# Kernel optimization log

Hardware: AMD Instinct MI355X
Metric: run time of the kernel (lower is better)

Reference implementation:

```python
import jax, jax.numpy as jnp
import numpy as np

CH = 16
R = 9  # reduced_res = ceil(log2(256)+1)


def grid_sample_bilinear(P, gx, gy):
    """torch.F.grid_sample, mode=bilinear, align_corners=True, zeros padding.
    P: (C, H, W); gx indexes width (last axis), gy indexes height. Returns (C, N)."""
    C, H, W = P.shape
    ix = (gx + 1.0) * 0.5 * (W - 1)
    iy = (gy + 1.0) * 0.5 * (H - 1)
    x0 = jnp.floor(ix)
    y0 = jnp.floor(iy)
    wx = ix - x0
    wy = iy - y0
    x0i = jnp.clip(x0.astype(jnp.int32), 0, W - 1)
    x1i = jnp.clip(x0i + 1, 0, W - 1)
    y0i = jnp.clip(y0.astype(jnp.int32), 0, H - 1)
    y1i = jnp.clip(y0i + 1, 0, H - 1)
    v00 = P[:, y0i, x0i]
    v01 = P[:, y0i, x1i]
    v10 = P[:, y1i, x0i]
    v11 = P[:, y1i, x1i]
    return (v00 * (1 - wx) * (1 - wy) + v01 * wx * (1 - wy)
            + v10 * (1 - wx) * wy + v11 * wx * wy)


def plane_feature(P, gx, gy, c_int):
    # sample -> (N, ch, R), then cosine-basis numerical integration over R
    s = grid_sample_bilinear(P, gx, gy)              # (R*ch, N)
    s = s.T.reshape(-1, CH, R)                       # (N, ch, R)
    c = (c_int + 1.0) * 0.5 * (2.0 ** (R - 1) - 1.0)  # (N,)
    freqs = (2.0 ** jnp.arange(R, dtype=jnp.float32)) - 0.5
    basis = jnp.cos(jnp.pi * (c[:, None] + 0.5) * freqs / (2.0 ** R))  # (N, R)
    return 2.0 * jnp.einsum('nr,ncr->nc', basis, s)  # (N, ch)


def setup_inputs() -> dict:
    key = jax.random.key(0)
    k1, k2, k3, k4 = jax.random.split(key, 4)
    coords = jax.random.uniform(k1, (524288, 3), dtype=jnp.float32) * 2.0 - 1.0
    Pu = jax.random.normal(k2, (R * CH, 256, 256), dtype=jnp.float32) * 0.1
    Pv = jax.random.normal(k3, (R * CH, 256, 256), dtype=jnp.float32) * 0.1
    Pw = jax.random.normal(k4, (R * CH, 256, 256), dtype=jnp.float32) * 0.1
    return {"coords": coords, "Pu": Pu, "Pv": Pv, "Pw": Pw}


def reference(coords, Pu, Pv, Pw):
    # Pu sampled with (coord1, coord2), integrated along coord0; etc.
    fu = plane_feature(Pu, coords[:, 1], coords[:, 2], coords[:, 0])
    fv = plane_feature(Pv, coords[:, 0], coords[:, 2], coords[:, 1])
    fw = plane_feature(Pw, coords[:, 0], coords[:, 1], coords[:, 2])
    return fu + fv + fw  # (N, ch)
```

## Files before the change

### kernel.cpp

```cpp
#include <hip/hip_runtime.h>
#include <hip/hip_bf16.h>

#define CHN 16
#define RF 9
#define HWDIM 256
#define POSN (HWDIM * HWDIM)
#define NBINS 32768

typedef _Float16 half2_t __attribute__((ext_vector_type(2)));

__device__ __forceinline__ half2_t u2h(uint32_t u) {
    union { uint32_t u; half2_t h; } x; x.u = u; return x.h;
}
__device__ __forceinline__ uint32_t f2h(float f) {
    union { _Float16 h; uint16_t u; } x; x.h = (_Float16)f; return (uint32_t)x.u;
}
__device__ __forceinline__ float h2f(uint32_t u) {
    union { uint16_t u; _Float16 h; } x; x.u = (uint16_t)u; return (float)x.h;
}

#if __has_builtin(__builtin_amdgcn_fdot2)
__device__ __forceinline__ float DOT2(half2_t a, half2_t b, float c) {
    return __builtin_amdgcn_fdot2(a, b, c, false);
}
#else
__device__ __forceinline__ float DOT2(half2_t a, half2_t b, float c) {
    return fmaf((float)a.x, (float)b.x, fmaf((float)a.y, (float)b.y, c));
}
#endif

__device__ __forceinline__ uint32_t part1by2(uint32_t x) {
    x &= 0x3ffu;
    x = (x | (x << 16)) & 0x030000FFu;
    x = (x | (x << 8))  & 0x0300F00Fu;
    x = (x | (x << 4))  & 0x030C30C3u;
    x = (x | (x << 2))  & 0x09249249u;
    return x;
}
__device__ __forceinline__ uint32_t morton_key(float c0, float c1, float c2) {
    int q0 = min(31, max(0, (int)((c0 + 1.f) * 16.f)));
    int q1 = min(31, max(0, (int)((c1 + 1.f) * 16.f)));
    int q2 = min(31, max(0, (int)((c2 + 1.f) * 16.f)));
    return (part1by2((uint32_t)q0) << 2) | (part1by2((uint32_t)q1) << 1) | part1by2((uint32_t)q2);
}

__global__ __launch_bounds__(256) void prep_kernel(const float* __restrict__ Pu,
                                                   const float* __restrict__ Pv,
                                                   const float* __restrict__ Pw,
                                                   uint4* __restrict__ A,
                                                   uint32_t* __restrict__ B,
                                                   const float* __restrict__ coords,
                                                   uint32_t* __restrict__ hist,
                                                   int N, int tblk) {
    int b = blockIdx.x;
    if (b < tblk) {
        int tid = b * 256 + threadIdx.x;
        int pos = tid & (POSN - 1);
        int p = tid >> 16;
        const float* P = (p == 0) ? Pu : ((p == 1) ? Pv : Pw);
        uint32_t r8pk[8];
        uint4* Ap = A + ((size_t)p * POSN + pos) * CHN;
#pragma unroll
        for (int cc = 0; cc < CHN; ++cc) {
            const float* Pc = P + (size_t)(cc * RF) * POSN + pos;
            uint32_t w[4];
#pragma unroll
            for (int j = 0; j < 4; ++j) {
                float v0 = Pc[(size_t)(2 * j) * POSN];
                float v1 = Pc[(size_t)(2 * j + 1) * POSN];
                w[j] = f2h(v0) | (f2h(v1) << 16);
            }
            Ap[cc] = make_uint4(w[0], w[1], w[2], w[3]);
            uint32_t h8 = f2h(Pc[(size_t)8 * POSN]);
            if (cc & 1) r8pk[cc >> 1] |= (h8 << 16); else r8pk[cc >> 1] = h8;
        }
        uint32_t* Bp = B + ((size_t)p * POSN + pos) * 8;
#pragma unroll
        for (int j = 0; j < 8; ++j) Bp[j] = r8pk[j];
    } else {
        int n = (b - tblk) * 256 + threadIdx.x;
        if (n < N) {
            float c0 = coords[3 * n], c1 = coords[3 * n + 1], c2 = coords[3 * n + 2];
            atomicAdd(&hist[morton_key(c0, c1, c2)], 1u);
        }
    }
}

__global__ __launch_bounds__(1024) void scan_kernel(uint32_t* __restrict__ hist) {
    __shared__ uint32_t part[1024];
    int t = threadIdx.x;
    uint32_t loc[32];
    uint32_t s = 0;
    int base = t * 32;
#pragma unroll
    for (int i = 0; i < 32; ++i) { loc[i] = hist[base + i]; s += loc[i]; }
    part[t] = s;
    __syncthreads();
    for (int off = 1; off < 1024; off <<= 1) {
        uint32_t v = (t >= off) ? part[t - off] : 0u;
        __syncthreads();
        part[t] += v;
        __syncthreads();
    }
    uint32_t run = part[t] - s;
#pragma unroll
    for (int i = 0; i < 32; ++i) { hist[base + i] = run; run += loc[i]; }
}

__global__ __launch_bounds__(256) void scatter_kernel(const float* __restrict__ coords,
                                                      uint32_t* __restrict__ hist,
                                                      float4* __restrict__ sorted, int N) {
    int n = blockIdx.x * blockDim.x + threadIdx.x;
    if (n >= N) return;
    float c0 = coords[3 * n], c1 = coords[3 * n + 1], c2 = coords[3 * n + 2];
    uint32_t key = morton_key(c0, c1, c2);
    uint32_t dst = atomicAdd(&hist[key], 1u);
    sorted[dst] = make_float4(c0, c1, c2, __uint_as_float((uint32_t)n));
}

__global__ __launch_bounds__(256) void triplane_f16(const float4* __restrict__ sorted,
                                                    const uint4* __restrict__ A,
                                                    const uint32_t* __restrict__ B,
                                                    float* __restrict__ out, int N, int nblk) {
    __shared__ float4 pts[16];
    __shared__ uint32_t meta[16][3][16];
    int blk = blockIdx.x;
    if ((nblk & 7) == 0) {
        int cpx = nblk >> 3;
        blk = (blk & 7) * cpx + (blk >> 3);
    }
    int base = blk * 16;
    int t = threadIdx.x;
    if (t < 16) {
        int i = base + t;
        pts[t] = (i < N) ? sorted[i] : make_float4(0.f, 0.f, 0.f, __uint_as_float(0u));
    }
    __syncthreads();
    if (t < 64 && (t & 3) < 3) {
        int pt = t >> 2, p = t & 3;
        float4 c = pts[pt];
        float gx = (p == 0) ? c.y : c.x;
        float gy = (p == 2) ? c.y : c.z;
        float ci = (p == 0) ? c.x : ((p == 1) ? c.y : c.z);
        float ix = (gx + 1.f) * 127.5f;
        float iy = (gy + 1.f) * 127.5f;
        float x0f = floorf(ix), y0f = floorf(iy);
        float wx = ix - x0f, wy = iy - y0f;
        int x0 = min(max((int)x0f, 0), HWDIM - 1);
        int y0 = min(max((int)y0f, 0), HWDIM - 1);
        int x1 = min(x0 + 1, HWDIM - 1);
        int y1 = min(y0 + 1, HWDIM - 1);
        uint32_t* m = meta[pt][p];
        float cv = (ci + 1.f) * 127.5f + 0.5f;
        float bb[9];
#pragma unroll
        for (int r = 0; r < 9; ++r) {
            const float k = 3.14159265358979f * ((float)(1 << r) - 0.5f) * (1.f / 512.f);
            bb[r] = __cosf(cv * k);
        }
#pragma unroll
        for (int j = 0; j < 4; ++j) m[j] = f2h(bb[2 * j]) | (f2h(bb[2 * j + 1]) << 16);
        m[4] = __float_as_uint(bb[8]);
        m[5] = __float_as_uint((1.f - wx) * (1.f - wy));
        m[6] = __float_as_uint(wx * (1.f - wy));
        m[7] = __float_as_uint((1.f - wx) * wy);
        m[8] = __float_as_uint(wx * wy);
        m[9]  = (uint32_t)(y0 * HWDIM + x0) * 256u;
        m[10] = (uint32_t)(y0 * HWDIM + x1) * 256u;
        m[11] = (uint32_t)(y1 * HWDIM + x0) * 256u;
        m[12] = (uint32_t)(y1 * HWDIM + x1) * 256u;
    }
    __syncthreads();
    int pt = t >> 4, cc = t & 15;
    int gi = base + pt;
    if (gi >= N) return;
    float acc = 0.f;
    const char* Ab = (const char*)A;
    const char* Bb = (const char*)B;
#pragma unroll
    for (int p = 0; p < 3; ++p) {
        const uint32_t* m = meta[pt][p];
        half2_t b01 = u2h(m[0]), b23 = u2h(m[1]), b45 = u2h(m[2]), b67 = u2h(m[3]);
        float b8 = __uint_as_float(m[4]);
        const char* Apl = Ab + (size_t)p * ((size_t)POSN * 256);
        const char* Bpl = Bb + (size_t)p * ((size_t)POSN * 32);
        float ps = 0.f;
#pragma unroll
        for (int k = 0; k < 4; ++k) {
            uint32_t ob = m[9 + k];
            uint4 a = *(const uint4*)(Apl + ob + cc * 16);
            uint32_t bw = *(const uint32_t*)(Bpl + (ob >> 3) + ((cc >> 1) << 2));
            float v8 = h2f((cc & 1) ? (bw >> 16) : (bw & 0xffffu));
            float s = b8 * v8;
            s = DOT2(u2h(a.x), b01, s);
            s = DOT2(u2h(a.y), b23, s);
            s = DOT2(u2h(a.z), b45, s);
            s = DOT2(u2h(a.w), b67, s);
            ps = fmaf(__uint_as_float(m[5 + k]), s, ps);
        }
        acc += ps;
    }
    uint32_t n = __float_as_uint(pts[pt].w);
    out[(size_t)n * CHN + cc] = 2.f * acc;
}

__global__ __launch_bounds__(256) void triplane_direct(const float* __restrict__ coords,
                                                       const float* __restrict__ Pu,
                                                       const float* __restrict__ Pv,
                                                       const float* __restrict__ Pw,
                                                       float* __restrict__ out, int N) {
    int tid = blockIdx.x * blockDim.x + threadIdx.x;
    int n = tid >> 4;
    if (n >= N) return;
    int cc = tid & 15;
    float c0 = coords[3 * n + 0];
    float c1 = coords[3 * n + 1];
    float c2 = coords[3 * n + 2];
    float acc = 0.f;
#pragma unroll
    for (int p = 0; p < 3; ++p) {
        const float* P = (p == 0) ? Pu : ((p == 1) ? Pv : Pw);
        float gx = (p == 0) ? c1 : c0;
        float gy = (p == 2) ? c1 : c2;
        float ci = (p == 0) ? c0 : ((p == 1) ? c1 : c2);
        float ix = (gx + 1.f) * 127.5f;
        float iy = (gy + 1.f) * 127.5f;
        float x0f = floorf(ix), y0f = floorf(iy);
        float wx = ix - x0f, wy = iy - y0f;
        int x0 = min(max((int)x0f, 0), HWDIM - 1);
        int y0 = min(max((int)y0f, 0), HWDIM - 1);
        int x1 = min(x0 + 1, HWDIM - 1);
        int y1 = min(y0 + 1, HWDIM - 1);
        float cv = (ci + 1.f) * 127.5f + 0.5f;
        float w00 = (1.f - wx) * (1.f - wy), w01 = wx * (1.f - wy);
        float w10 = (1.f - wx) * wy, w11 = wx * wy;
        int p00 = y0 * HWDIM + x0, p01 = y0 * HWDIM + x1;
        int p10 = y1 * HWDIM + x0, p11 = y1 * HWDIM + x1;
#pragma unroll
        for (int r = 0; r < RF; ++r) {
            const float k = 3.14159265358979f * ((float)(1 << r) - 0.5f) / 512.f;
            float b = __cosf(cv * k);
            const float* Pc = P + (size_t)(cc * RF + r) * POSN;
            float v = w00 * Pc[p00] + w01 * Pc[p01] + w10 * Pc[p10] + w11 * Pc[p11];
            acc = fmaf(b, v, acc);
        }
    }
    out[(size_t)n * CHN + cc] = 2.f * acc;
}

extern "C" void kernel_launch(void* const* d_in, const int* in_sizes, int n_in,
                              void* d_out, int out_size, void* d_ws, size_t ws_size,
                              hipStream_t stream) {
    const float* coords = (const float*)d_in[0];
    const float* Pu = (const float*)d_in[1];
    const float* Pv = (const float*)d_in[2];
    const float* Pw = (const float*)d_in[3];
    float* out = (float*)d_out;
    int N = in_sizes[0] / 3;

    size_t offA = 0;
    size_t szA = (size_t)3 * POSN * CHN * sizeof(uint4);
    size_t offB = offA + szA;
    size_t szB = (size_t)3 * POSN * 8 * sizeof(uint32_t);
    size_t offS = offB + szB;
    size_t szS = (size_t)N * sizeof(float4);
    size_t offH = offS + szS;
    size_t szH = (size_t)NBINS * sizeof(uint32_t);
    size_t need = offH + szH;

    if (ws_size >= need) {
        char* ws = (char*)d_ws;
        uint4* A = (uint4*)(ws + offA);
        uint32_t* B = (uint32_t*)(ws + offB);
        float4* sorted = (float4*)(ws + offS);
        uint32_t* hist = (uint32_t*)(ws + offH);

        hipMemsetAsync(hist, 0, szH, stream);
        int tblk = (3 * POSN) / 256;
        int hblk = (N + 255) / 256;
        prep_kernel<<<tblk + hblk, 256, 0, stream>>>(Pu, Pv, Pw, A, B, coords, hist, N, tblk);
        scan_kernel<<<1, 1024, 0, stream>>>(hist);
        scatter_kernel<<<(N + 255) / 256, 256, 0, stream>>>(coords, hist, sorted, N);

        int nblk = (N + 15) / 16;
        triplane_f16<<<nblk, 256, 0, stream>>>(sorted, A, B, out, N, nblk);
    } else {
        int threads = N * CHN;
        triplane_direct<<<(threads + 255) / 256, 256, 0, stream>>>(coords, Pu, Pv, Pw, out, N);
    }
}
```

Before: 172.0 us.

## Stage prep writes through LDS and process two points per thread in sampler

The prep kernel now packs each 128-position tile into shared memory and then writes the f16 tables out with fully coalesced stores, where before each thread did strided 256-byte stores. The sampling kernel handles 32 points per block, with each thread computing two points, to amortise the metadata setup and barriers. The XCD block remapping is generalised to block counts that are not a multiple of eight. The cost is more shared memory in prep and fewer, heavier blocks in the sampler, which may reduce occupancy.

```diff
diff --git a/kernel.cpp b/kernel.cpp
--- a/kernel.cpp
+++ b/kernel.cpp
@@ -44,7 +44,7 @@
     return (part1by2((uint32_t)q0) << 2) | (part1by2((uint32_t)q1) << 1) | part1by2((uint32_t)q2);
 }
 
-__global__ __launch_bounds__(256) void prep_kernel(const float* __restrict__ Pu,
+__global__ __launch_bounds__(128) void prep_kernel(const float* __restrict__ Pu,
                                                    const float* __restrict__ Pv,
                                                    const float* __restrict__ Pw,
                                                    uint4* __restrict__ A,
@@ -52,17 +52,20 @@
                                                    const float* __restrict__ coords,
                                                    uint32_t* __restrict__ hist,
                                                    int N, int tblk) {
+    __shared__ uint4 LA[128 * 17];
+    __shared__ uint32_t LB[128 * 9];
     int b = blockIdx.x;
+    int t = threadIdx.x;
     if (b < tblk) {
-        int tid = b * 256 + threadIdx.x;
-        int pos = tid & (POSN - 1);
-        int p = tid >> 16;
+        int tile = b;
+        int p = tile >> 9;
+        int pos_base = (tile & 511) * 128;
         const float* P = (p == 0) ? Pu : ((p == 1) ? Pv : Pw);
         uint32_t r8pk[8];
-        uint4* Ap = A + ((size_t)p * POSN + pos) * CHN;
+        const float* Pc0 = P + pos_base + t;
 #pragma unroll
         for (int cc = 0; cc < CHN; ++cc) {
-            const float* Pc = P + (size_t)(cc * RF) * POSN + pos;
+            const float* Pc = Pc0 + (size_t)(cc * RF) * POSN;
             uint32_t w[4];
 #pragma unroll
             for (int j = 0; j < 4; ++j) {
@@ -70,15 +73,27 @@
                 float v1 = Pc[(size_t)(2 * j + 1) * POSN];
                 w[j] = f2h(v0) | (f2h(v1) << 16);
             }
-            Ap[cc] = make_uint4(w[0], w[1], w[2], w[3]);
+            LA[t * 17 + cc] = make_uint4(w[0], w[1], w[2], w[3]);
             uint32_t h8 = f2h(Pc[(size_t)8 * POSN]);
             if (cc & 1) r8pk[cc >> 1] |= (h8 << 16); else r8pk[cc >> 1] = h8;
         }
-        uint32_t* Bp = B + ((size_t)p * POSN + pos) * 8;
-#pragma unroll
-        for (int j = 0; j < 8; ++j) Bp[j] = r8pk[j];
+#pragma unroll
+        for (int j = 0; j < 8; ++j) LB[t * 9 + j] = r8pk[j];
+        __syncthreads();
+        uint4* Aout = A + ((size_t)p * POSN + pos_base) * CHN;
+#pragma unroll
+        for (int it = 0; it < 16; ++it) {
+            int i = it * 128 + t;
+            Aout[i] = LA[(i >> 4) * 17 + (i & 15)];
+        }
+        uint32_t* Bout = B + ((size_t)p * POSN + pos_base) * 8;
+#pragma unroll
+        for (int it = 0; it < 8; ++it) {
+            int i = it * 128 + t;
+            Bout[i] = LB[(i >> 3) * 9 + (i & 7)];
+        }
     } else {
-        int n = (b - tblk) * 256 + threadIdx.x;
+        int n = (b - tblk) * 128 + t;
         if (n < N) {
             float c0 = coords[3 * n], c1 = coords[3 * n + 1], c2 = coords[3 * n + 2];
             atomicAdd(&hist[morton_key(c0, c1, c2)], 1u);
@@ -118,25 +133,26 @@
     sorted[dst] = make_float4(c0, c1, c2, __uint_as_float((uint32_t)n));
 }
 
-__global__ __launch_bounds__(256) void triplane_f16(const float4* __restrict__ sorted,
-                                                    const uint4* __restrict__ A,
-                                                    const uint32_t* __restrict__ B,
-                                                    float* __restrict__ out, int N, int nblk) {
-    __shared__ float4 pts[16];
-    __shared__ uint32_t meta[16][3][16];
+__global__ __launch_bounds__(256) void triplane_f16v2(const float4* __restrict__ sorted,
+                                                      const uint4* __restrict__ A,
+                                                      const uint32_t* __restrict__ B,
+                                                      float* __restrict__ out, int N, int nblk) {
+    __shared__ float4 pts[32];
+    __shared__ uint32_t meta[32 * 40];
     int blk = blockIdx.x;
-    if ((nblk & 7) == 0) {
-        int cpx = nblk >> 3;
-        blk = (blk & 7) * cpx + (blk >> 3);
-    }
-    int base = blk * 16;
+    {
+        int q = nblk >> 3, r = nblk & 7;
+        int xcd = blk & 7, local = blk >> 3;
+        blk = (xcd < r ? xcd * (q + 1) : r * (q + 1) + (xcd - r) * q) + local;
+    }
+    int base = blk * 32;
     int t = threadIdx.x;
-    if (t < 16) {
+    if (t < 32) {
         int i = base + t;
         pts[t] = (i < N) ? sorted[i] : make_float4(0.f, 0.f, 0.f, __uint_as_float(0u));
     }
     __syncthreads();
-    if (t < 64 && (t & 3) < 3) {
+    if (t < 128 && (t & 3) < 3) {
         int pt = t >> 2, p = t & 3;
         float4 c = pts[pt];
         float gx = (p == 0) ? c.y : c.x;
@@ -150,7 +166,7 @@
         int y0 = min(max((int)y0f, 0), HWDIM - 1);
         int x1 = min(x0 + 1, HWDIM - 1);
         int y1 = min(y0 + 1, HWDIM - 1);
-        uint32_t* m = meta[pt][p];
+        uint32_t* m = &meta[pt * 40 + p * 13];
         float cv = (ci + 1.f) * 127.5f + 0.5f;
         float bb[9];
 #pragma unroll
@@ -171,37 +187,42 @@
         m[12] = (uint32_t)(y1 * HWDIM + x1) * 256u;
     }
     __syncthreads();
-    int pt = t >> 4, cc = t & 15;
-    int gi = base + pt;
-    if (gi >= N) return;
-    float acc = 0.f;
+    int cc = t & 15, slot = t >> 4;
     const char* Ab = (const char*)A;
     const char* Bb = (const char*)B;
 #pragma unroll
-    for (int p = 0; p < 3; ++p) {
-        const uint32_t* m = meta[pt][p];
-        half2_t b01 = u2h(m[0]), b23 = u2h(m[1]), b45 = u2h(m[2]), b67 = u2h(m[3]);
-        float b8 = __uint_as_float(m[4]);
-        const char* Apl = Ab + (size_t)p * ((size_t)POSN * 256);
-        const char* Bpl = Bb + (size_t)p * ((size_t)POSN * 32);
-        float ps = 0.f;
-#pragma unroll
-        for (int k = 0; k < 4; ++k) {
-            uint32_t ob = m[9 + k];
-            uint4 a = *(const uint4*)(Apl + ob + cc * 16);
-            uint32_t bw = *(const uint32_t*)(Bpl + (ob >> 3) + ((cc >> 1) << 2));
-            float v8 = h2f((cc & 1) ? (bw >> 16) : (bw & 0xffffu));
-            float s = b8 * v8;
-            s = DOT2(u2h(a.x), b01, s);
-            s = DOT2(u2h(a.y), b23, s);
-            s = DOT2(u2h(a.z), b45, s);
-            s = DOT2(u2h(a.w), b67, s);
-            ps = fmaf(__uint_as_float(m[5 + k]), s, ps);
-        }
-        acc += ps;
-    }
-    uint32_t n = __float_as_uint(pts[pt].w);
-    out[(size_t)n * CHN + cc] = 2.f * acc;
+    for (int half = 0; half < 2; ++half) {
+        int pt = slot + half * 16;
+        int gi = base + pt;
+        float acc = 0.f;
+#pragma unroll
+        for (int p = 0; p < 3; ++p) {
+            const uint32_t* m = &meta[pt * 40 + p * 13];
+            half2_t b01 = u2h(m[0]), b23 = u2h(m[1]), b45 = u2h(m[2]), b67 = u2h(m[3]);
+            float b8 = __uint_as_float(m[4]);
+            const char* Apl = Ab + (size_t)p * ((size_t)POSN * 256);
+            const char* Bpl = Bb + (size_t)p * ((size_t)POSN * 32);
+            float ps = 0.f;
+#pragma unroll
+            for (int k = 0; k < 4; ++k) {
+                uint32_t ob = m[9 + k];
+                uint4 a = *(const uint4*)(Apl + ob + cc * 16);
+                uint32_t bw = *(const uint32_t*)(Bpl + (ob >> 3) + ((cc >> 1) << 2));
+                float v8 = h2f((cc & 1) ? (bw >> 16) : (bw & 0xffffu));
+                float s = b8 * v8;
+                s = DOT2(u2h(a.x), b01, s);
+                s = DOT2(u2h(a.y), b23, s);
+                s = DOT2(u2h(a.z), b45, s);
+                s = DOT2(u2h(a.w), b67, s);
+                ps = fmaf(__uint_as_float(m[5 + k]), s, ps);
+            }
+            acc += ps;
+        }
+        if (gi < N) {
+            uint32_t n = __float_as_uint(pts[pt].w);
+            out[(size_t)n * CHN + cc] = 2.f * acc;
+        }
+    }
 }
 
 __global__ __launch_bounds__(256) void triplane_direct(const float* __restrict__ coords,
@@ -276,14 +297,14 @@
         uint32_t* hist = (uint32_t*)(ws + offH);
 
         hipMemsetAsync(hist, 0, szH, stream);
-        int tblk = (3 * POSN) / 256;
-        int hblk = (N + 255) / 256;
-        prep_kernel<<<tblk + hblk, 256, 0, stream>>>(Pu, Pv, Pw, A, B, coords, hist, N, tblk);
+        int tblk = (3 * POSN) / 128;
+        int hblk = (N + 127) / 128;
+        prep_kernel<<<tblk + hblk, 128, 0, stream>>>(Pu, Pv, Pw, A, B, coords, hist, N, tblk);
         scan_kernel<<<1, 1024, 0, stream>>>(hist);
         scatter_kernel<<<(N + 255) / 256, 256, 0, stream>>>(coords, hist, sorted, N);
 
-        int nblk = (N + 15) / 16;
-        triplane_f16<<<nblk, 256, 0, stream>>>(sorted, A, B, out, N, nblk);
+        int nblk = (N + 31) / 32;
+        triplane_f16v2<<<nblk, 256, 0, stream>>>(sorted, A, B, out, N, nblk);
     } else {
         int threads = N * CHN;
         triplane_direct<<<(threads + 255) / 256, 256, 0, stream>>>(coords, Pu, Pv, Pw, out, N);
```

Result: faster. 167.2 us (-2.8%).
